# Kernel optimization log

Measured on AMD Instinct MI355X. Metric: run time of the kernel, lower is better.

The kernel has to match this reference:

```python
import jax, jax.numpy as jnp
import numpy as np

N = 30000      # nodes
E = 300000     # edges (before self-loops)
G = 1024       # graphs
D_IN = 256     # embedding dim
HID = 256      # hidden dim
H = 8          # heads
C = HID // H   # per-head dim
VOCAB = 65


def setup_inputs() -> dict:
    key = jax.random.key(0)
    ks = jax.random.split(key, 32)
    inp = {
        "x_ids": jax.random.randint(ks[0], (N,), 0, VOCAB),
        "edge_index": jax.random.randint(ks[1], (2, E), 0, N),
        "batch_ids": (jnp.arange(N) * G) // N,  # sorted graph ids, every graph non-empty
        "emb": jax.random.normal(ks[2], (VOCAB, D_IN)) * 0.05,
        "fw": jax.random.normal(ks[3], (1, HID)) * 0.05,
        "fb": jnp.zeros((1,)),
    }
    k = 4
    for i, d_in in enumerate([D_IN, HID, HID, HID, HID], start=1):
        inp[f"W{i}"] = jax.random.normal(ks[k], (HID, d_in)) * (1.0 / np.sqrt(d_in)); k += 1
        inp[f"as{i}"] = jax.random.normal(ks[k], (H, C)) * 0.1; k += 1
        inp[f"ad{i}"] = jax.random.normal(ks[k], (H, C)) * 0.1; k += 1
        inp[f"b{i}"] = jnp.zeros((HID,))
    return inp


def _gat_conv(x, src, dst, W, a_src, a_dst, b):
    # x: [N, d_in] -> h: [N, H, C]
    h = (x @ W.T).reshape(N, H, C)
    e_src = jnp.einsum("nhc,hc->nh", h, a_src)  # [N, H]
    e_dst = jnp.einsum("nhc,hc->nh", h, a_dst)
    e = jax.nn.leaky_relu(e_src[src] + e_dst[dst], 0.2)  # [E', H]
    m = jax.ops.segment_max(e, dst, num_segments=N)      # segment softmax over incoming edges
    ex = jnp.exp(e - m[dst])
    s = jax.ops.segment_sum(ex, dst, num_segments=N)
    alpha = ex / (s[dst] + 1e-16)                        # [E', H]
    out = jax.ops.segment_sum(h[src] * alpha[:, :, None], dst, num_segments=N)
    return out.reshape(N, H * C) + b


def reference(x_ids, edge_index, batch_ids, emb,
              W1, as1, ad1, b1, W2, as2, ad2, b2, W3, as3, ad3, b3,
              W4, as4, ad4, b4, W5, as5, ad5, b5, fw, fb):
    # Embedding with max_norm=1: rescale looked-up rows whose L2 norm exceeds 1
    x = emb[x_ids]
    nrm = jnp.linalg.norm(x, axis=-1, keepdims=True)
    x = x * jnp.minimum(1.0, 1.0 / (nrm + 1e-12))
    # add self-loops once (PyG GATConv default)
    loop = jnp.arange(N)
    src = jnp.concatenate([edge_index[0], loop])
    dst = jnp.concatenate([edge_index[1], loop])
    x = jax.nn.relu(_gat_conv(x, src, dst, W1, as1, ad1, b1))
    x = jax.nn.relu(_gat_conv(x, src, dst, W2, as2, ad2, b2))
    x = jax.nn.relu(_gat_conv(x, src, dst, W3, as3, ad3, b3))
    x = jax.nn.relu(_gat_conv(x, src, dst, W4, as4, ad4, b4))
    x = jax.nn.relu(_gat_conv(x, src, dst, W5, as5, ad5, b5))
    pooled = jax.ops.segment_max(x, batch_ids, num_segments=G)  # [G, HID]
    return (pooled @ fw.T + fb).reshape(-1)  # [G]
```

## Files before the change

kernel.cpp:

```cpp
#include <hip/hip_runtime.h>
#include <float.h>
#include <math.h>

constexpr int NN  = 30000;
constexpr int EE  = 300000;
constexpr int GG  = 1024;
constexpr int HID = 256;
constexpr int NH  = 8;
constexpr int EP  = EE + NN;
constexpr int NP  = 30080;

typedef short bf16x8 __attribute__((ext_vector_type(8)));
typedef float f32x4 __attribute__((ext_vector_type(4)));

__device__ __forceinline__ void gload_lds16(const void* g, void* l) {
    __builtin_amdgcn_global_load_lds(
        (const __attribute__((address_space(1))) unsigned int*)g,
        (__attribute__((address_space(3))) unsigned int*)l, 16, 0, 0);
}

__device__ __forceinline__ void f2hilo(float x, unsigned short& h, unsigned short& l) {
    unsigned u = __float_as_uint(x);
    h = (unsigned short)(u >> 16);
    float hv = __uint_as_float(u & 0xFFFF0000u);
    float r = x - hv;
    unsigned v = __float_as_uint(r);
    unsigned rnd = ((v >> 16) & 1u) + 0x7FFFu;
    l = (unsigned short)((v + rnd) >> 16);
}

__device__ __forceinline__ float bf2f(unsigned short u) {
    return __uint_as_float(((unsigned)u) << 16);
}

__device__ __forceinline__ unsigned fmap(float x) {
    unsigned b = __float_as_uint(x);
    return (b & 0x80000000u) ? ~b : (b | 0x80000000u);
}
__device__ __forceinline__ float funmap(unsigned u) {
    return (u & 0x80000000u) ? __uint_as_float(u ^ 0x80000000u) : __uint_as_float(~u);
}

__global__ void k_hist(const int* __restrict__ edst, int* __restrict__ cnt) {
    int i = blockIdx.x * blockDim.x + threadIdx.x;
    if (i >= EP) return;
    int d = (i < EE) ? edst[i] : (i - EE);
    atomicAdd(&cnt[d], 1);
}

__global__ void k_scan(const int* __restrict__ cnt, int* __restrict__ indptr) {
    __shared__ int wtot[16];
    __shared__ int carry_s;
    int tid = threadIdx.x;
    int lane = tid & 63, wid = tid >> 6;
    if (tid == 0) carry_s = 0;
    __syncthreads();
    for (int base = 0; base < NN; base += 1024) {
        int i = base + tid;
        int v = (i < NN) ? cnt[i] : 0;
        int incl = v;
        #pragma unroll
        for (int off = 1; off < 64; off <<= 1) {
            int t = __shfl_up(incl, off, 64);
            if (lane >= off) incl += t;
        }
        if (lane == 63) wtot[wid] = incl;
        __syncthreads();
        int wpre = 0;
        for (int w = 0; w < wid; ++w) wpre += wtot[w];
        int c = carry_s;
        if (i < NN) indptr[i] = c + wpre + incl - v;
        int tot = 0;
        for (int w = 0; w < 16; ++w) tot += wtot[w];
        __syncthreads();
        if (tid == 0) carry_s = c + tot;
        __syncthreads();
    }
    if (tid == 0) indptr[NN] = carry_s;
}

__global__ void k_fill(const int* __restrict__ esrc, const int* __restrict__ edst,
                       const int* __restrict__ indptr, int* __restrict__ cursor,
                       int* __restrict__ srcs) {
    int i = blockIdx.x * blockDim.x + threadIdx.x;
    if (i >= EP) return;
    int d, s;
    if (i < EE) { d = edst[i]; s = esrc[i]; } else { d = i - EE; s = i - EE; }
    int pos = indptr[d] + atomicAdd(&cursor[d], 1);
    srcs[pos] = s;
}

__global__ void k_sortseg(int* __restrict__ srcs, const int* __restrict__ indptr) {
    int node = blockIdx.x * blockDim.x + threadIdx.x;
    if (node >= NN) return;
    int b = indptr[node], e = indptr[node + 1];
    for (int i = b + 1; i < e; ++i) {
        int v = srcs[i];
        int j = i - 1;
        while (j >= b && srcs[j] > v) { srcs[j + 1] = srcs[j]; --j; }
        srcs[j + 1] = v;
    }
}

__global__ void k_starts(const int* __restrict__ batch, int* __restrict__ starts) {
    int i = blockIdx.x * blockDim.x + threadIdx.x;
    if (i >= NN) return;
    int b = batch[i];
    if (i == 0 || batch[i - 1] != b) starts[b] = i;
    if (i == NN - 1) starts[GG] = NN;
}

__global__ void k_wconv(const float* __restrict__ W1, const float* __restrict__ W2,
                        const float* __restrict__ W3, const float* __restrict__ W4,
                        const float* __restrict__ W5,
                        unsigned short* __restrict__ Whi, unsigned short* __restrict__ Wlo) {
    int i = blockIdx.x * blockDim.x + threadIdx.x;
    int l = blockIdx.y;
    const float* W = (l == 0) ? W1 : (l == 1) ? W2 : (l == 2) ? W3 : (l == 3) ? W4 : W5;
    unsigned short h, lo;
    f2hilo(W[i], h, lo);
    Whi[(size_t)l * 65536 + i] = h;
    Wlo[(size_t)l * 65536 + i] = lo;
}

__global__ void k_embed(const int* __restrict__ ids, const float* __restrict__ emb,
                        unsigned short* __restrict__ Phi, unsigned short* __restrict__ Plo) {
    int w = (blockIdx.x * blockDim.x + threadIdx.x) >> 6;
    if (w >= NN) return;
    int lane = threadIdx.x & 63;
    const float4 v = *(const float4*)(emb + (size_t)ids[w] * HID + lane * 4);
    float ss = v.x * v.x + v.y * v.y + v.z * v.z + v.w * v.w;
    #pragma unroll
    for (int off = 32; off >= 1; off >>= 1) ss += __shfl_xor(ss, off, 64);
    float nrm = sqrtf(ss);
    float sc = fminf(1.0f, 1.0f / (nrm + 1e-12f));
    float o[4] = {v.x * sc, v.y * sc, v.z * sc, v.w * sc};
    ushort4 hv, lv;
    f2hilo(o[0], hv.x, lv.x); f2hilo(o[1], hv.y, lv.y);
    f2hilo(o[2], hv.z, lv.z); f2hilo(o[3], hv.w, lv.w);
    *(ushort4*)(Phi + (size_t)w * HID + lane * 4) = hv;
    *(ushort4*)(Plo + (size_t)w * HID + lane * 4) = lv;
}

__global__ __launch_bounds__(256) void k_gemm(const unsigned short* __restrict__ Ahi,
                                              const unsigned short* __restrict__ Alo,
                                              const unsigned short* __restrict__ Bhi,
                                              const unsigned short* __restrict__ Blo,
                                              const float* __restrict__ a_src,
                                              const float* __restrict__ a_dst,
                                              float* __restrict__ O,
                                              float* __restrict__ es,
                                              float* __restrict__ ed, int M) {
    __shared__ unsigned short lds[4][128 * 64];
    const int tid = threadIdx.x;
    const int m0 = blockIdx.x * 128;
    const int n0 = blockIdx.y * 128;
    const int wid = tid >> 6, lane = tid & 63;
    const int wm = wid >> 1, wn = wid & 1;
    const int r16 = lane & 15, kq = lane >> 4;

    f32x4 acc[4][4];
    #pragma unroll
    for (int i = 0; i < 4; ++i)
        #pragma unroll
        for (int j = 0; j < 4; ++j) acc[i][j] = (f32x4){0.f, 0.f, 0.f, 0.f};

    for (int kt = 0; kt < 4; ++kt) {
        const int kk = kt * 64;
        #pragma unroll
        for (int rnd = 0; rnd < 4; ++rnd) {
            int q = rnd * 256 + tid;
            int row = q >> 3, c = q & 7;
            int sc = c ^ (row & 7);
            size_t goffA = (size_t)(m0 + row) * HID + kk + sc * 8;
            size_t goffB = (size_t)(n0 + row) * HID + kk + sc * 8;
            gload_lds16(Ahi + goffA, &lds[0][q * 8]);
            gload_lds16(Alo + goffA, &lds[1][q * 8]);
            gload_lds16(Bhi + goffB, &lds[2][q * 8]);
            gload_lds16(Blo + goffB, &lds[3][q * 8]);
        }
        __syncthreads();
        #pragma unroll
        for (int ks = 0; ks < 2; ++ks) {
            bf16x8 ah[4], al[4], bh[4], bl[4];
            #pragma unroll
            for (int f = 0; f < 4; ++f) {
                int rowa = wm * 64 + f * 16 + r16;
                int ca = (ks * 4 + kq) ^ (rowa & 7);
                int offa = rowa * 64 + ca * 8;
                ah[f] = *(const bf16x8*)&lds[0][offa];
                al[f] = *(const bf16x8*)&lds[1][offa];
                int rowb = wn * 64 + f * 16 + r16;
                int cb = (ks * 4 + kq) ^ (rowb & 7);
                int offb = rowb * 64 + cb * 8;
                bh[f] = *(const bf16x8*)&lds[2][offb];
                bl[f] = *(const bf16x8*)&lds[3][offb];
            }
            #pragma unroll
            for (int mi = 0; mi < 4; ++mi)
                #pragma unroll
                for (int ni = 0; ni < 4; ++ni) {
                    acc[mi][ni] = __builtin_amdgcn_mfma_f32_16x16x32_bf16(ah[mi], bh[ni], acc[mi][ni], 0, 0, 0);
                    acc[mi][ni] = __builtin_amdgcn_mfma_f32_16x16x32_bf16(ah[mi], bl[ni], acc[mi][ni], 0, 0, 0);
                    acc[mi][ni] = __builtin_amdgcn_mfma_f32_16x16x32_bf16(al[mi], bh[ni], acc[mi][ni], 0, 0, 0);
                }
        }
        __syncthreads();
    }
    const int headA = (n0 >> 5) + wn * 2;
    const float asA0 = a_src[headA * 32 + r16],      asA1 = a_src[headA * 32 + 16 + r16];
    const float asB0 = a_src[headA * 32 + 32 + r16], asB1 = a_src[headA * 32 + 48 + r16];
    const float adA0 = a_dst[headA * 32 + r16],      adA1 = a_dst[headA * 32 + 16 + r16];
    const float adB0 = a_dst[headA * 32 + 32 + r16], adB1 = a_dst[headA * 32 + 48 + r16];
    #pragma unroll
    for (int mi = 0; mi < 4; ++mi) {
        #pragma unroll
        for (int q = 0; q < 4; ++q) {
            int row = m0 + wm * 64 + mi * 16 + kq * 4 + q;
            float ps0 = acc[mi][0][q] * asA0 + acc[mi][1][q] * asA1;
            float ps1 = acc[mi][2][q] * asB0 + acc[mi][3][q] * asB1;
            float pd0 = acc[mi][0][q] * adA0 + acc[mi][1][q] * adA1;
            float pd1 = acc[mi][2][q] * adB0 + acc[mi][3][q] * adB1;
            #pragma unroll
            for (int off = 1; off < 16; off <<= 1) {
                ps0 += __shfl_xor(ps0, off, 16);
                ps1 += __shfl_xor(ps1, off, 16);
                pd0 += __shfl_xor(pd0, off, 16);
                pd1 += __shfl_xor(pd1, off, 16);
            }
            if (row < M) {
                #pragma unroll
                for (int ni = 0; ni < 4; ++ni)
                    O[(size_t)row * HID + n0 + wn * 64 + ni * 16 + r16] = acc[mi][ni][q];
                if (r16 == 0) {
                    es[row * NH + headA]     = ps0;
                    es[row * NH + headA + 1] = ps1;
                    ed[row * NH + headA]     = pd0;
                    ed[row * NH + headA + 1] = pd1;
                }
            }
        }
    }
}

__global__ void k_edge(const int* __restrict__ eidx, const float* __restrict__ es,
                       const float* __restrict__ ed, float* __restrict__ elog,
                       unsigned* __restrict__ mU) {
    int t = blockIdx.x * blockDim.x + threadIdx.x;
    if (t >= EP * NH) return;
    int j = t >> 3, h = t & 7;
    int s, d;
    if (j < EE) { s = eidx[j]; d = eidx[EE + j]; } else { s = j - EE; d = s; }
    float e = es[s * NH + h] + ed[d * NH + h];
    e = (e > 0.f) ? e : 0.2f * e;
    elog[t] = e;
    atomicMax(&mU[d * NH + h], fmap(e));
}

__global__ __launch_bounds__(256) void k_aggregate(const float* __restrict__ H,
                                                   const float* __restrict__ elog,
                                                   const unsigned* __restrict__ mU,
                                                   const int* __restrict__ indptr,
                                                   const int* __restrict__ srcs,
                                                   const float* __restrict__ bias,
                                                   unsigned short* __restrict__ Phi,
                                                   unsigned short* __restrict__ Plo) {
    int node = (blockIdx.x * blockDim.x + threadIdx.x) >> 6;
    if (node >= NN) return;
    int lane = threadIdx.x & 63;
    int head = lane >> 3;
    int b0 = indptr[node], e0 = indptr[node + 1];
    float m = funmap(mU[node * NH + head]);
    float4 a0 = {0.f, 0.f, 0.f, 0.f}, a1 = a0, a2 = a0, a3 = a0;
    float s0 = 0.f, s1 = 0.f, s2 = 0.f, s3 = 0.f;
    int j = b0;
    for (; j + 3 < e0; j += 4) {
        int x0 = srcs[j], x1 = srcs[j + 1], x2 = srcs[j + 2], x3 = srcs[j + 3];
        float ev0 = elog[(size_t)(j + 0) * NH + head];
        float ev1 = elog[(size_t)(j + 1) * NH + head];
        float ev2 = elog[(size_t)(j + 2) * NH + head];
        float ev3 = elog[(size_t)(j + 3) * NH + head];
        float4 h0 = *(const float4*)(H + (size_t)x0 * HID + lane * 4);
        float4 h1 = *(const float4*)(H + (size_t)x1 * HID + lane * 4);
        float4 h2 = *(const float4*)(H + (size_t)x2 * HID + lane * 4);
        float4 h3 = *(const float4*)(H + (size_t)x3 * HID + lane * 4);
        float w0 = expf(ev0 - m), w1 = expf(ev1 - m);
        float w2 = expf(ev2 - m), w3 = expf(ev3 - m);
        s0 += w0; s1 += w1; s2 += w2; s3 += w3;
        a0.x = fmaf(w0, h0.x, a0.x); a0.y = fmaf(w0, h0.y, a0.y);
        a0.z = fmaf(w0, h0.z, a0.z); a0.w = fmaf(w0, h0.w, a0.w);
        a1.x = fmaf(w1, h1.x, a1.x); a1.y = fmaf(w1, h1.y, a1.y);
        a1.z = fmaf(w1, h1.z, a1.z); a1.w = fmaf(w1, h1.w, a1.w);
        a2.x = fmaf(w2, h2.x, a2.x); a2.y = fmaf(w2, h2.y, a2.y);
        a2.z = fmaf(w2, h2.z, a2.z); a2.w = fmaf(w2, h2.w, a2.w);
        a3.x = fmaf(w3, h3.x, a3.x); a3.y = fmaf(w3, h3.y, a3.y);
        a3.z = fmaf(w3, h3.z, a3.z); a3.w = fmaf(w3, h3.w, a3.w);
    }
    for (; j < e0; ++j) {
        int x0 = srcs[j];
        float ev = elog[(size_t)j * NH + head];
        float4 h0 = *(const float4*)(H + (size_t)x0 * HID + lane * 4);
        float w0 = expf(ev - m);
        s0 += w0;
        a0.x = fmaf(w0, h0.x, a0.x); a0.y = fmaf(w0, h0.y, a0.y);
        a0.z = fmaf(w0, h0.z, a0.z); a0.w = fmaf(w0, h0.w, a0.w);
    }
    float sum = (s0 + s1) + (s2 + s3);
    float ax = (a0.x + a1.x) + (a2.x + a3.x);
    float ay = (a0.y + a1.y) + (a2.y + a3.y);
    float az = (a0.z + a1.z) + (a2.z + a3.z);
    float aw = (a0.w + a1.w) + (a2.w + a3.w);
    float inv = 1.f / (sum + 1e-16f);
    float4 bv = *(const float4*)(bias + lane * 4);
    float o[4];
    o[0] = fmaxf(fmaf(ax, inv, bv.x), 0.f);
    o[1] = fmaxf(fmaf(ay, inv, bv.y), 0.f);
    o[2] = fmaxf(fmaf(az, inv, bv.z), 0.f);
    o[3] = fmaxf(fmaf(aw, inv, bv.w), 0.f);
    ushort4 hv, lv;
    f2hilo(o[0], hv.x, lv.x); f2hilo(o[1], hv.y, lv.y);
    f2hilo(o[2], hv.z, lv.z); f2hilo(o[3], hv.w, lv.w);
    *(ushort4*)(Phi + (size_t)node * HID + lane * 4) = hv;
    *(ushort4*)(Plo + (size_t)node * HID + lane * 4) = lv;
}

__global__ void k_pool(const unsigned short* __restrict__ Phi,
                       const unsigned short* __restrict__ Plo,
                       const int* __restrict__ starts,
                       const float* __restrict__ fw, const float* __restrict__ fb,
                       float* __restrict__ out) {
    int g = (blockIdx.x * blockDim.x + threadIdx.x) >> 6;
    if (g >= GG) return;
    int lane = threadIdx.x & 63;
    int s = starts[g], e = starts[g + 1];
    float mx0 = -FLT_MAX, mx1 = -FLT_MAX, mx2 = -FLT_MAX, mx3 = -FLT_MAX;
    for (int n = s; n < e; ++n) {
        ushort4 hv = *(const ushort4*)(Phi + (size_t)n * HID + lane * 4);
        ushort4 lv = *(const ushort4*)(Plo + (size_t)n * HID + lane * 4);
        mx0 = fmaxf(mx0, bf2f(hv.x) + bf2f(lv.x));
        mx1 = fmaxf(mx1, bf2f(hv.y) + bf2f(lv.y));
        mx2 = fmaxf(mx2, bf2f(hv.z) + bf2f(lv.z));
        mx3 = fmaxf(mx3, bf2f(hv.w) + bf2f(lv.w));
    }
    float4 w = *(const float4*)(fw + lane * 4);
    float t = mx0 * w.x + mx1 * w.y + mx2 * w.z + mx3 * w.w;
    #pragma unroll
    for (int off = 32; off >= 1; off >>= 1) t += __shfl_xor(t, off, 64);
    if (lane == 0) out[g] = t + fb[0];
}

extern "C" void kernel_launch(void* const* d_in, const int* in_sizes, int n_in,
                              void* d_out, int out_size, void* d_ws, size_t ws_size,
                              hipStream_t stream) {
    const int* x_ids = (const int*)d_in[0];
    const int* eidx  = (const int*)d_in[1];
    const int* batch = (const int*)d_in[2];
    const float* emb = (const float*)d_in[3];
    const float* fw  = (const float*)d_in[4];
    const float* fb  = (const float*)d_in[5];
    const float* Wl[5], *asl[5], *adl[5], *bl[5];
    for (int l = 0; l < 5; ++l) {
        Wl[l]  = (const float*)d_in[6 + 4 * l];
        asl[l] = (const float*)d_in[7 + 4 * l];
        adl[l] = (const float*)d_in[8 + 4 * l];
        bl[l]  = (const float*)d_in[9 + 4 * l];
    }

    char* ws = (char*)d_ws;
    size_t off = 0;
    auto alloc = [&](size_t bytes) {
        void* p = ws + off;
        off = (off + bytes + 255) & ~(size_t)255;
        return p;
    };
    unsigned short* Phi = (unsigned short*)alloc((size_t)NP * HID * 2);
    unsigned short* Plo = (unsigned short*)alloc((size_t)NP * HID * 2);
    float* Q    = (float*)alloc((size_t)NN * HID * 4);
    unsigned short* Whi = (unsigned short*)alloc((size_t)5 * HID * HID * 2);
    unsigned short* Wlo = (unsigned short*)alloc((size_t)5 * HID * HID * 2);
    float* es   = (float*)alloc((size_t)NN * NH * 4);
    float* ed   = (float*)alloc((size_t)NN * NH * 4);
    float* elog = (float*)alloc((size_t)EP * NH * 4);
    unsigned* mU = (unsigned*)alloc((size_t)5 * NN * NH * 4);
    int* cnt    = (int*)alloc((size_t)NN * 4);
    int* cursor = (int*)alloc((size_t)NN * 4);
    int* indptr = (int*)alloc((size_t)(NN + 1) * 4);
    int* srcs   = (int*)alloc((size_t)EP * 4);
    int* starts = (int*)alloc((size_t)(GG + 1) * 4);
    (void)ws_size; (void)in_sizes; (void)n_in; (void)out_size;

    hipMemsetAsync(cnt, 0, (size_t)NN * 4, stream);
    hipMemsetAsync(cursor, 0, (size_t)NN * 4, stream);
    hipMemsetAsync(mU, 0, (size_t)5 * NN * NH * 4, stream);

    k_hist<<<(EP + 255) / 256, 256, 0, stream>>>(eidx + EE, cnt);
    k_scan<<<1, 1024, 0, stream>>>(cnt, indptr);
    k_fill<<<(EP + 255) / 256, 256, 0, stream>>>(eidx, eidx + EE, indptr, cursor, srcs);
    k_sortseg<<<(NN + 255) / 256, 256, 0, stream>>>(srcs, indptr);
    k_starts<<<(NN + 255) / 256, 256, 0, stream>>>(batch, starts);
    k_wconv<<<dim3(HID * HID / 256, 5), 256, 0, stream>>>(Wl[0], Wl[1], Wl[2], Wl[3], Wl[4], Whi, Wlo);
    k_embed<<<NN / 4, 256, 0, stream>>>(x_ids, emb, Phi, Plo);

    for (int l = 0; l < 5; ++l) {
        unsigned* mUl = mU + (size_t)l * NN * NH;
        dim3 gg(NP / 128, HID / 128);
        k_gemm<<<gg, 256, 0, stream>>>(Phi, Plo, Whi + (size_t)l * HID * HID,
                                       Wlo + (size_t)l * HID * HID,
                                       asl[l], adl[l], Q, es, ed, NN);
        k_edge<<<(EP * NH + 255) / 256, 256, 0, stream>>>(eidx, es, ed, elog, mUl);
        k_aggregate<<<NN / 4, 256, 0, stream>>>(Q, elog, mUl, indptr, srcs, bl[l], Phi, Plo);
    }
    k_pool<<<GG / 4, 256, 0, stream>>>(Phi, Plo, starts, fw, fb, (float*)d_out);
}
```

Measured before the change: 599.5 us.

## Precompute attention-projected weights and compute scores in previous layer's epilogue

New measurement: 727.9 us. 1.21x slower.

```diff
diff --git a/kernel.cpp b/kernel.cpp
--- a/kernel.cpp
+++ b/kernel.cpp
@@ -39,6 +39,24 @@
 }
 __device__ __forceinline__ float funmap(unsigned u) {
     return (u & 0x80000000u) ? __uint_as_float(u ^ 0x80000000u) : __uint_as_float(~u);
+}
+
+__device__ __forceinline__ void score_epilogue(const float* __restrict__ wt,
+                                               const float o[4], int lane, int node,
+                                               float* __restrict__ es,
+                                               float* __restrict__ ed) {
+    float acc[16];
+    #pragma unroll
+    for (int t = 0; t < 16; ++t) {
+        const float4 w = *(const float4*)(wt + t * 256 + lane * 4);
+        acc[t] = o[0] * w.x + o[1] * w.y + o[2] * w.z + o[3] * w.w;
+    }
+    #pragma unroll
+    for (int off = 1; off < 64; off <<= 1)
+        #pragma unroll
+        for (int t = 0; t < 16; ++t) acc[t] += __shfl_xor(acc[t], off, 64);
+    if (lane < 8) es[node * NH + lane] = acc[lane * 2];
+    else if (lane < 16) ed[node * NH + (lane - 8)] = acc[(lane - 8) * 2 + 1];
 }
 
 __global__ void k_hist(const int* __restrict__ edst, int* __restrict__ cnt) {
@@ -90,7 +108,8 @@
     srcs[pos] = s;
 }
 
-__global__ void k_sortseg(int* __restrict__ srcs, const int* __restrict__ indptr) {
+__global__ void k_sortseg(int* __restrict__ srcs, const int* __restrict__ indptr,
+                          int* __restrict__ dsts) {
     int node = blockIdx.x * blockDim.x + threadIdx.x;
     if (node >= NN) return;
     int b = indptr[node], e = indptr[node + 1];
@@ -100,6 +119,7 @@
         while (j >= b && srcs[j] > v) { srcs[j + 1] = srcs[j]; --j; }
         srcs[j + 1] = v;
     }
+    for (int i = b; i < e; ++i) dsts[i] = node;
 }
 
 __global__ void k_starts(const int* __restrict__ batch, int* __restrict__ starts) {
@@ -123,8 +143,22 @@
     Wlo[(size_t)l * 65536 + i] = lo;
 }
 
+__global__ void k_wtilde(const float* __restrict__ W, const float* __restrict__ as,
+                         const float* __restrict__ ad, float* __restrict__ Wt) {
+    int t = blockIdx.x;
+    int k = threadIdx.x;
+    int h = t >> 1, type = t & 1;
+    const float* a = type ? ad : as;
+    float v = 0.f;
+    for (int c = 0; c < 32; ++c)
+        v = fmaf(a[h * 32 + c], W[(size_t)(h * 32 + c) * HID + k], v);
+    Wt[t * 256 + k] = v;
+}
+
 __global__ void k_embed(const int* __restrict__ ids, const float* __restrict__ emb,
-                        unsigned short* __restrict__ Phi, unsigned short* __restrict__ Plo) {
+                        const float* __restrict__ wt,
+                        unsigned short* __restrict__ Phi, unsigned short* __restrict__ Plo,
+                        float* __restrict__ es, float* __restrict__ ed) {
     int w = (blockIdx.x * blockDim.x + threadIdx.x) >> 6;
     if (w >= NN) return;
     int lane = threadIdx.x & 63;
@@ -140,17 +174,14 @@
     f2hilo(o[2], hv.z, lv.z); f2hilo(o[3], hv.w, lv.w);
     *(ushort4*)(Phi + (size_t)w * HID + lane * 4) = hv;
     *(ushort4*)(Plo + (size_t)w * HID + lane * 4) = lv;
+    score_epilogue(wt, o, lane, w, es, ed);
 }
 
 __global__ __launch_bounds__(256) void k_gemm(const unsigned short* __restrict__ Ahi,
                                               const unsigned short* __restrict__ Alo,
                                               const unsigned short* __restrict__ Bhi,
                                               const unsigned short* __restrict__ Blo,
-                                              const float* __restrict__ a_src,
-                                              const float* __restrict__ a_dst,
-                                              float* __restrict__ O,
-                                              float* __restrict__ es,
-                                              float* __restrict__ ed, int M) {
+                                              float* __restrict__ O, int M) {
     __shared__ unsigned short lds[4][128 * 64];
     const int tid = threadIdx.x;
     const int m0 = blockIdx.x * 128;
@@ -207,50 +238,27 @@
         }
         __syncthreads();
     }
-    const int headA = (n0 >> 5) + wn * 2;
-    const float asA0 = a_src[headA * 32 + r16],      asA1 = a_src[headA * 32 + 16 + r16];
-    const float asB0 = a_src[headA * 32 + 32 + r16], asB1 = a_src[headA * 32 + 48 + r16];
-    const float adA0 = a_dst[headA * 32 + r16],      adA1 = a_dst[headA * 32 + 16 + r16];
-    const float adB0 = a_dst[headA * 32 + 32 + r16], adB1 = a_dst[headA * 32 + 48 + r16];
     #pragma unroll
     for (int mi = 0; mi < 4; ++mi) {
         #pragma unroll
         for (int q = 0; q < 4; ++q) {
             int row = m0 + wm * 64 + mi * 16 + kq * 4 + q;
-            float ps0 = acc[mi][0][q] * asA0 + acc[mi][1][q] * asA1;
-            float ps1 = acc[mi][2][q] * asB0 + acc[mi][3][q] * asB1;
-            float pd0 = acc[mi][0][q] * adA0 + acc[mi][1][q] * adA1;
-            float pd1 = acc[mi][2][q] * adB0 + acc[mi][3][q] * adB1;
-            #pragma unroll
-            for (int off = 1; off < 16; off <<= 1) {
-                ps0 += __shfl_xor(ps0, off, 16);
-                ps1 += __shfl_xor(ps1, off, 16);
-                pd0 += __shfl_xor(pd0, off, 16);
-                pd1 += __shfl_xor(pd1, off, 16);
-            }
             if (row < M) {
                 #pragma unroll
                 for (int ni = 0; ni < 4; ++ni)
                     O[(size_t)row * HID + n0 + wn * 64 + ni * 16 + r16] = acc[mi][ni][q];
-                if (r16 == 0) {
-                    es[row * NH + headA]     = ps0;
-                    es[row * NH + headA + 1] = ps1;
-                    ed[row * NH + headA]     = pd0;
-                    ed[row * NH + headA + 1] = pd1;
-                }
             }
         }
     }
 }
 
-__global__ void k_edge(const int* __restrict__ eidx, const float* __restrict__ es,
-                       const float* __restrict__ ed, float* __restrict__ elog,
-                       unsigned* __restrict__ mU) {
+__global__ void k_edge(const int* __restrict__ srcs, const int* __restrict__ dsts,
+                       const float* __restrict__ es, const float* __restrict__ ed,
+                       float* __restrict__ elog, unsigned* __restrict__ mU) {
     int t = blockIdx.x * blockDim.x + threadIdx.x;
     if (t >= EP * NH) return;
     int j = t >> 3, h = t & 7;
-    int s, d;
-    if (j < EE) { s = eidx[j]; d = eidx[EE + j]; } else { s = j - EE; d = s; }
+    int s = srcs[j], d = dsts[j];
     float e = es[s * NH + h] + ed[d * NH + h];
     e = (e > 0.f) ? e : 0.2f * e;
     elog[t] = e;
@@ -263,53 +271,48 @@
                                                    const int* __restrict__ indptr,
                                                    const int* __restrict__ srcs,
                                                    const float* __restrict__ bias,
+                                                   const float* __restrict__ wt,
                                                    unsigned short* __restrict__ Phi,
-                                                   unsigned short* __restrict__ Plo) {
+                                                   unsigned short* __restrict__ Plo,
+                                                   float* __restrict__ es,
+                                                   float* __restrict__ ed) {
     int node = (blockIdx.x * blockDim.x + threadIdx.x) >> 6;
     if (node >= NN) return;
     int lane = threadIdx.x & 63;
     int head = lane >> 3;
     int b0 = indptr[node], e0 = indptr[node + 1];
     float m = funmap(mU[node * NH + head]);
-    float4 a0 = {0.f, 0.f, 0.f, 0.f}, a1 = a0, a2 = a0, a3 = a0;
-    float s0 = 0.f, s1 = 0.f, s2 = 0.f, s3 = 0.f;
+    float4 a[8];
+    float s[8];
+    #pragma unroll
+    for (int u = 0; u < 8; ++u) { a[u] = (float4){0.f, 0.f, 0.f, 0.f}; s[u] = 0.f; }
     int j = b0;
-    for (; j + 3 < e0; j += 4) {
-        int x0 = srcs[j], x1 = srcs[j + 1], x2 = srcs[j + 2], x3 = srcs[j + 3];
-        float ev0 = elog[(size_t)(j + 0) * NH + head];
-        float ev1 = elog[(size_t)(j + 1) * NH + head];
-        float ev2 = elog[(size_t)(j + 2) * NH + head];
-        float ev3 = elog[(size_t)(j + 3) * NH + head];
-        float4 h0 = *(const float4*)(H + (size_t)x0 * HID + lane * 4);
-        float4 h1 = *(const float4*)(H + (size_t)x1 * HID + lane * 4);
-        float4 h2 = *(const float4*)(H + (size_t)x2 * HID + lane * 4);
-        float4 h3 = *(const float4*)(H + (size_t)x3 * HID + lane * 4);
-        float w0 = expf(ev0 - m), w1 = expf(ev1 - m);
-        float w2 = expf(ev2 - m), w3 = expf(ev3 - m);
-        s0 += w0; s1 += w1; s2 += w2; s3 += w3;
-        a0.x = fmaf(w0, h0.x, a0.x); a0.y = fmaf(w0, h0.y, a0.y);
-        a0.z = fmaf(w0, h0.z, a0.z); a0.w = fmaf(w0, h0.w, a0.w);
-        a1.x = fmaf(w1, h1.x, a1.x); a1.y = fmaf(w1, h1.y, a1.y);
-        a1.z = fmaf(w1, h1.z, a1.z); a1.w = fmaf(w1, h1.w, a1.w);
-        a2.x = fmaf(w2, h2.x, a2.x); a2.y = fmaf(w2, h2.y, a2.y);
-        a2.z = fmaf(w2, h2.z, a2.z); a2.w = fmaf(w2, h2.w, a2.w);
-        a3.x = fmaf(w3, h3.x, a3.x); a3.y = fmaf(w3, h3.y, a3.y);
-        a3.z = fmaf(w3, h3.z, a3.z); a3.w = fmaf(w3, h3.w, a3.w);
+    for (; j + 7 < e0; j += 8) {
+        #pragma unroll
+        for (int u = 0; u < 8; ++u) {
+            int x = srcs[j + u];
+            float ev = elog[(size_t)(j + u) * NH + head];
+            float4 hv = *(const float4*)(H + (size_t)x * HID + lane * 4);
+            float w = expf(ev - m);
+            s[u] += w;
+            a[u].x = fmaf(w, hv.x, a[u].x); a[u].y = fmaf(w, hv.y, a[u].y);
+            a[u].z = fmaf(w, hv.z, a[u].z); a[u].w = fmaf(w, hv.w, a[u].w);
+        }
     }
     for (; j < e0; ++j) {
-        int x0 = srcs[j];
+        int x = srcs[j];
         float ev = elog[(size_t)j * NH + head];
-        float4 h0 = *(const float4*)(H + (size_t)x0 * HID + lane * 4);
-        float w0 = expf(ev - m);
-        s0 += w0;
-        a0.x = fmaf(w0, h0.x, a0.x); a0.y = fmaf(w0, h0.y, a0.y);
-        a0.z = fmaf(w0, h0.z, a0.z); a0.w = fmaf(w0, h0.w, a0.w);
-    }
-    float sum = (s0 + s1) + (s2 + s3);
-    float ax = (a0.x + a1.x) + (a2.x + a3.x);
-    float ay = (a0.y + a1.y) + (a2.y + a3.y);
-    float az = (a0.z + a1.z) + (a2.z + a3.z);
-    float aw = (a0.w + a1.w) + (a2.w + a3.w);
+        float4 hv = *(const float4*)(H + (size_t)x * HID + lane * 4);
+        float w = expf(ev - m);
+        s[0] += w;
+        a[0].x = fmaf(w, hv.x, a[0].x); a[0].y = fmaf(w, hv.y, a[0].y);
+        a[0].z = fmaf(w, hv.z, a[0].z); a[0].w = fmaf(w, hv.w, a[0].w);
+    }
+    float sum = ((s[0] + s[1]) + (s[2] + s[3])) + ((s[4] + s[5]) + (s[6] + s[7]));
+    float ax = ((a[0].x + a[1].x) + (a[2].x + a[3].x)) + ((a[4].x + a[5].x) + (a[6].x + a[7].x));
+    float ay = ((a[0].y + a[1].y) + (a[2].y + a[3].y)) + ((a[4].y + a[5].y) + (a[6].y + a[7].y));
+    float az = ((a[0].z + a[1].z) + (a[2].z + a[3].z)) + ((a[4].z + a[5].z) + (a[6].z + a[7].z));
+    float aw = ((a[0].w + a[1].w) + (a[2].w + a[3].w)) + ((a[4].w + a[5].w) + (a[6].w + a[7].w));
     float inv = 1.f / (sum + 1e-16f);
     float4 bv = *(const float4*)(bias + lane * 4);
     float o[4];
@@ -322,6 +325,7 @@
     f2hilo(o[2], hv.z, lv.z); f2hilo(o[3], hv.w, lv.w);
     *(ushort4*)(Phi + (size_t)node * HID + lane * 4) = hv;
     *(ushort4*)(Plo + (size_t)node * HID + lane * 4) = lv;
+    if (wt) score_epilogue(wt, o, lane, node, es, ed);
 }
 
 __global__ void k_pool(const unsigned short* __restrict__ Phi,
@@ -378,6 +382,7 @@
     float* Q    = (float*)alloc((size_t)NN * HID * 4);
     unsigned short* Whi = (unsigned short*)alloc((size_t)5 * HID * HID * 2);
     unsigned short* Wlo = (unsigned short*)alloc((size_t)5 * HID * HID * 2);
+    float* Wt   = (float*)alloc((size_t)5 * 16 * HID * 4);
     float* es   = (float*)alloc((size_t)NN * NH * 4);
     float* ed   = (float*)alloc((size_t)NN * NH * 4);
     float* elog = (float*)alloc((size_t)EP * NH * 4);
@@ -386,6 +391,7 @@
     int* cursor = (int*)alloc((size_t)NN * 4);
     int* indptr = (int*)alloc((size_t)(NN + 1) * 4);
     int* srcs   = (int*)alloc((size_t)EP * 4);
+    int* dsts   = (int*)alloc((size_t)EP * 4);
     int* starts = (int*)alloc((size_t)(GG + 1) * 4);
     (void)ws_size; (void)in_sizes; (void)n_in; (void)out_size;
 
@@ -396,19 +402,21 @@
     k_hist<<<(EP + 255) / 256, 256, 0, stream>>>(eidx + EE, cnt);
     k_scan<<<1, 1024, 0, stream>>>(cnt, indptr);
     k_fill<<<(EP + 255) / 256, 256, 0, stream>>>(eidx, eidx + EE, indptr, cursor, srcs);
-    k_sortseg<<<(NN + 255) / 256, 256, 0, stream>>>(srcs, indptr);
+    k_sortseg<<<(NN + 255) / 256, 256, 0, stream>>>(srcs, indptr, dsts);
     k_starts<<<(NN + 255) / 256, 256, 0, stream>>>(batch, starts);
     k_wconv<<<dim3(HID * HID / 256, 5), 256, 0, stream>>>(Wl[0], Wl[1], Wl[2], Wl[3], Wl[4], Whi, Wlo);
-    k_embed<<<NN / 4, 256, 0, stream>>>(x_ids, emb, Phi, Plo);
+    for (int l = 0; l < 5; ++l)
+        k_wtilde<<<16, 256, 0, stream>>>(Wl[l], asl[l], adl[l], Wt + (size_t)l * 16 * HID);
+    k_embed<<<NN / 4, 256, 0, stream>>>(x_ids, emb, Wt, Phi, Plo, es, ed);
 
     for (int l = 0; l < 5; ++l) {
         unsigned* mUl = mU + (size_t)l * NN * NH;
+        k_edge<<<(EP * NH + 255) / 256, 256, 0, stream>>>(srcs, dsts, es, ed, elog, mUl);
         dim3 gg(NP / 128, HID / 128);
         k_gemm<<<gg, 256, 0, stream>>>(Phi, Plo, Whi + (size_t)l * HID * HID,
-                                       Wlo + (size_t)l * HID * HID,
-                                       asl[l], adl[l], Q, es, ed, NN);
-        k_edge<<<(EP * NH + 255) / 256, 256, 0, stream>>>(eidx, es, ed, elog, mUl);
-        k_aggregate<<<NN / 4, 256, 0, stream>>>(Q, elog, mUl, indptr, srcs, bl[l], Phi, Plo);
+                                       Wlo + (size_t)l * HID * HID, Q, NN);
+        const float* wtn = (l < 4) ? (Wt + (size_t)(l + 1) * 16 * HID) : nullptr;
+        k_aggregate<<<NN / 4, 256, 0, stream>>>(Q, elog, mUl, indptr, srcs, bl[l], wtn, Phi, Plo, es, ed);
     }
     k_pool<<<GG / 4, 256, 0, stream>>>(Phi, Plo, starts, fw, fb, (float*)d_out);
 }
```
